# Performance work log

Measured on AMD Instinct MI355X. Metric: run time of the kernel, lower is better.

Reference implementation:

```python
import jax, jax.numpy as jnp
import numpy as np

B, N, D, H, L, R = 2, 1024, 128, 8, 8, 4
HD = D // H            # head dim = 16
DH = int(D * 2.0)      # mlp hidden (mlp_ratio=2.0)
TWO_R = 2 * R
LS_INIT = 1e-3


def _ln(x, g, b):
    m = x.mean(-1, keepdims=True)
    v = ((x - m) ** 2).mean(-1, keepdims=True)
    return (x - m) / jnp.sqrt(v + 1e-5) * g + b


def _gelu(t):
    return jax.nn.gelu(t, approximate=False)  # torch nn.GELU default (erf)


def _attn(x, mask, bias, qkv_w, proj_w, proj_b, w_pre, w_post):
    Bx, Nx, C = x.shape
    qkv = (x @ qkv_w.T).reshape(Bx, Nx, 3, H, HD).transpose(2, 0, 3, 1, 4)
    q, k, v = qkv[0], qkv[1], qkv[2]               # each [B,H,N,hd]
    a = jnp.einsum('bhid,bhjd->bhij', q, k) * (HD ** -0.5)
    a = a + mask[:, None] + bias                   # pairwise mask + rbf/edge bias
    a = jnp.einsum('bhij,gh->bgij', a, w_pre)      # talk-head pre-softmax
    a = jax.nn.softmax(a, axis=-1)
    a = jnp.einsum('bhij,gh->bgij', a, w_post)     # talk-head post-softmax
    o = jnp.einsum('bhij,bhjd->bihd', a, v).reshape(Bx, Nx, C)
    return o @ proj_w.T + proj_b


def setup_inputs() -> dict:
    key = jax.random.key(0)
    ks = jax.random.split(key, 16)
    s = 0.02
    x = jax.random.normal(ks[0], (B, N, D), jnp.float32)
    dist = jax.random.uniform(ks[1], (B, N, N), jnp.float32) * 20.0
    attn_mask = jnp.where(jax.random.uniform(ks[2], (B, N, N)) < 0.02, -1e4, 0.0).astype(jnp.float32)
    local_mask = jnp.where(dist > 8.0, -1e4, 0.0).astype(jnp.float32)
    edge_type = jax.random.randint(ks[3], (B, N, N), 0, 4)
    return {
        'x': x, 'dist': dist, 'attn_mask': attn_mask, 'local_mask': local_mask,
        'edge_type': edge_type,
        'ln_g': jnp.ones((L, 3, D), jnp.float32), 'ln_b': jnp.zeros((L, 3, D), jnp.float32),
        'qkv_w': jax.random.normal(ks[4], (L, 2, 3 * D, D), jnp.float32) * s,
        'proj_w': jax.random.normal(ks[5], (L, 2, D, D), jnp.float32) * s,
        'proj_b': jnp.zeros((L, 2, D), jnp.float32),
        'th_pre': jnp.eye(H, dtype=jnp.float32) + jax.random.normal(ks[6], (L, 2, H, H), jnp.float32) * s,
        'th_post': jnp.eye(H, dtype=jnp.float32) + jax.random.normal(ks[7], (L, 2, H, H), jnp.float32) * s,
        'ls': jnp.full((L, 3, D), LS_INIT, jnp.float32),
        'fc1_w': jax.random.normal(ks[8], (L, DH, D), jnp.float32) * s,
        'fc1_b': jnp.zeros((L, DH), jnp.float32),
        'fc2_w': jax.random.normal(ks[9], (L, D, DH), jnp.float32) * s,
        'fc2_b': jnp.zeros((L, D), jnp.float32),
        'de_ln_g': jnp.ones((L, TWO_R), jnp.float32), 'de_ln_b': jnp.zeros((L, TWO_R), jnp.float32),
        'de_w': jax.random.normal(ks[10], (L, H, TWO_R), jnp.float32) * 0.5,
        'de_b': jnp.zeros((L, H), jnp.float32),
        'edge_emb': jax.random.normal(ks[11], (L, 4, R), jnp.float32) * 0.5,
        'rbf_mu': jnp.linspace(0.0, 20.0, R).astype(jnp.float32),
        'rbf_sigma': jnp.full((R,), 20.0 / R, jnp.float32),
    }


def reference(x, dist, attn_mask, local_mask, edge_type, ln_g, ln_b, qkv_w, proj_w,
              proj_b, th_pre, th_post, ls, fc1_w, fc1_b, fc2_w, fc2_b,
              de_ln_g, de_ln_b, de_w, de_b, edge_emb, rbf_mu, rbf_sigma):
    # RBF features of pairwise distances: [B,N,N,R] (mu/sigma buffers shared across layers)
    rbf = jnp.exp(-(((dist[..., None] - rbf_mu) / rbf_sigma) ** 2))
    first_mask = attn_mask + local_mask  # num_dist_mask == 1
    for l in range(L):
        feat = jnp.concatenate([rbf, edge_emb[l][edge_type]], axis=-1)  # [B,N,N,2R]
        bias = _gelu(_ln(feat, de_ln_g[l], de_ln_b[l]) @ de_w[l].T + de_b[l])  # [B,N,N,H]
        bias = jnp.moveaxis(bias, -1, 1)  # [B,H,N,N]
        x = x + ls[l, 0] * _attn(_ln(x, ln_g[l, 0], ln_b[l, 0]), first_mask, bias,
                                 qkv_w[l, 0], proj_w[l, 0], proj_b[l, 0], th_pre[l, 0], th_post[l, 0])
        x = x + ls[l, 1] * _attn(_ln(x, ln_g[l, 1], ln_b[l, 1]), attn_mask, bias,
                                 qkv_w[l, 1], proj_w[l, 1], proj_b[l, 1], th_pre[l, 1], th_post[l, 1])
        h = _ln(x, ln_g[l, 2], ln_b[l, 2])
        h = _gelu(h @ fc1_w[l].T + fc1_b[l]) @ fc2_w[l].T + fc2_b[l]
        x = x + ls[l, 2] * h
    return x
```

## Files before the change

kernel.cpp:

```cpp
#include <hip/hip_runtime.h>
#include <math.h>

#define BB 2
#define NN 1024
#define DD 128
#define HH 8
#define NL 8
#define RR 4
#define DHID 256
#define TWO_R 8
#define MM (BB*NN)
#define TB 2048

typedef __attribute__((ext_vector_type(8))) short short8;
typedef __attribute__((ext_vector_type(4))) float f32x4;

__device__ __forceinline__ float gelu_erf(float x) {
    return 0.5f * x * (1.0f + erff(x * 0.70710678118654752f));
}
__device__ __forceinline__ ushort f2b(float f) {
    union { float f; unsigned u; } v; v.f = f;
    return (ushort)((v.u + 0x7FFFu + ((v.u >> 16) & 1u)) >> 16);
}
__device__ __forceinline__ float b2f(ushort u) {
    union { unsigned u; float f; } v; v.u = ((unsigned)u) << 16;
    return v.f;
}
__device__ __forceinline__ unsigned pk2(float a, float b) {
    return ((unsigned)f2b(b) << 16) | (unsigned)f2b(a);
}

__global__ __launch_bounds__(256) void cvt4_kernel(
    const float* __restrict__ s0, int n0, const float* __restrict__ s1, int n1,
    const float* __restrict__ s2, int n2, const float* __restrict__ s3, int n3,
    ushort* __restrict__ d0, ushort* __restrict__ d1,
    ushort* __restrict__ d2, ushort* __restrict__ d3) {
    int t = blockIdx.x * 256 + threadIdx.x;
    if (t < n0) { d0[t] = f2b(s0[t]); return; } t -= n0;
    if (t < n1) { d1[t] = f2b(s1[t]); return; } t -= n1;
    if (t < n2) { d2[t] = f2b(s2[t]); return; } t -= n2;
    if (t < n3) { d3[t] = f2b(s3[t]); }
}

__global__ __launch_bounds__(256) void maskprep_kernel(
    const float* __restrict__ am, const float* __restrict__ lm,
    ushort* __restrict__ fmask, ushort* __restrict__ amask) {
    int t = blockIdx.x * 256 + threadIdx.x;
    if (t >= BB * NN * NN) return;
    float a = am[t];
    amask[t] = f2b(a);
    fmask[t] = f2b(a + lm[t]);
}

__global__ __launch_bounds__(256) void table_kernel(
    const float* __restrict__ de_ln_g, const float* __restrict__ de_ln_b,
    const float* __restrict__ de_w, const float* __restrict__ de_b,
    const float* __restrict__ edge_emb, const float* __restrict__ mu,
    const float* __restrict__ sigma, float* __restrict__ tab) {
    int t = blockIdx.x * 256 + threadIdx.x;
    if (t >= NL * 4 * TB) return;
    int idx = t & (TB - 1);
    int et = (t >> 11) & 3;
    int l = t >> 13;
    float d = idx * (20.0f / (float)(TB - 1));
    float f[8];
#pragma unroll
    for (int r = 0; r < RR; ++r) {
        float u = (d - mu[r]) / sigma[r];
        f[r] = expf(-u * u);
    }
#pragma unroll
    for (int r = 0; r < RR; ++r) f[4 + r] = edge_emb[(l * 4 + et) * RR + r];
    float m = 0.f;
#pragma unroll
    for (int r = 0; r < 8; ++r) m += f[r];
    m *= 0.125f;
    float v = 0.f;
#pragma unroll
    for (int r = 0; r < 8; ++r) { float dd = f[r] - m; v += dd * dd; }
    v *= 0.125f;
    float inv = rsqrtf(v + 1e-5f);
    float fn[8];
#pragma unroll
    for (int r = 0; r < 8; ++r)
        fn[r] = (f[r] - m) * inv * de_ln_g[l * 8 + r] + de_ln_b[l * 8 + r];
#pragma unroll
    for (int h = 0; h < HH; ++h) {
        float z = de_b[l * 8 + h];
#pragma unroll
        for (int r = 0; r < 8; ++r) z += de_w[(l * 8 + h) * 8 + r] * fn[r];
        tab[(size_t)t * 8 + h] = gelu_erf(z);
    }
}

#define GF_BIAS 1
#define GF_GELU 2
#define GF_RESID 4
#define GF_OUTBF 8

template <int AMODE, int FLAGS, int KDIM>
__global__ __launch_bounds__(256) void gemm_mfma(
    const void* __restrict__ Ain, const ushort* __restrict__ W,
    const float* __restrict__ bias, const float* __restrict__ ls,
    const float* __restrict__ resid, const float* __restrict__ lng,
    const float* __restrict__ lnb, void* __restrict__ out, int Nd) {
    __shared__ ushort As[64][KDIM + 8];
    __shared__ ushort Ws[64][KDIM + 8];
    int tid = threadIdx.x;
    int bm = blockIdx.x, bn = blockIdx.y;
    if (AMODE == 1) {
        int r = tid >> 2, c = tid & 3;
        const float* xr = (const float*)Ain + (size_t)(bm * 64 + r) * 128 + c * 32;
        float v[32];
        float s = 0.f, ss = 0.f;
#pragma unroll
        for (int k = 0; k < 8; ++k) {
            float4 f = ((const float4*)xr)[k];
            v[4 * k] = f.x; v[4 * k + 1] = f.y; v[4 * k + 2] = f.z; v[4 * k + 3] = f.w;
            s += f.x + f.y + f.z + f.w;
            ss += f.x * f.x + f.y * f.y + f.z * f.z + f.w * f.w;
        }
        s += __shfl_xor(s, 1, 64);  s += __shfl_xor(s, 2, 64);
        ss += __shfl_xor(ss, 1, 64); ss += __shfl_xor(ss, 2, 64);
        float mean = s * (1.f / 128.f);
        float var = ss * (1.f / 128.f) - mean * mean;
        float inv = rsqrtf(var + 1e-5f);
        unsigned* dst = (unsigned*)&As[r][c * 32];
#pragma unroll
        for (int k = 0; k < 16; ++k) {
            int col = c * 32 + 2 * k;
            float a0 = (v[2 * k] - mean) * inv * lng[col] + lnb[col];
            float a1 = (v[2 * k + 1] - mean) * inv * lng[col + 1] + lnb[col + 1];
            dst[k] = pk2(a0, a1);
        }
    } else if (AMODE == 2) {
        const float* Apart = (const float*)Ain;
        for (int v = tid; v < 64 * 32; v += 256) {
            int r = v >> 5, c = v & 31;
            size_t off = (size_t)(bm * 64 + r) * 128 + c * 4;
            float4 s0 = *(const float4*)(Apart + off);
            float4 s1 = *(const float4*)(Apart + (size_t)MM * 128 + off);
            unsigned* dst = (unsigned*)&As[r][c * 4];
            dst[0] = pk2(s0.x + s1.x, s0.y + s1.y);
            dst[1] = pk2(s0.z + s1.z, s0.w + s1.w);
        }
    } else {
        const ushort* A = (const ushort*)Ain;
        for (int v = tid; v < 64 * KDIM / 8; v += 256) {
            int r = v / (KDIM / 8), c = v % (KDIM / 8);
            *(short8*)&As[r][c * 8] =
                *(const short8*)(A + (size_t)(bm * 64 + r) * KDIM + c * 8);
        }
    }
    for (int v = tid; v < 64 * KDIM / 8; v += 256) {
        int r = v / (KDIM / 8), c = v % (KDIM / 8);
        *(short8*)&Ws[r][c * 8] =
            *(const short8*)(W + (size_t)(bn * 64 + r) * KDIM + c * 8);
    }
    __syncthreads();
    int wv = tid >> 6, l = tid & 63;
    int wm = (wv >> 1) * 32, wn = (wv & 1) * 32;
    int lr = l & 15, lk = (l >> 4) * 8;
    f32x4 acc[2][2] = {};
#pragma unroll
    for (int k0 = 0; k0 < KDIM; k0 += 32) {
        short8 af[2], bf[2];
        af[0] = *(const short8*)&As[wm + lr][k0 + lk];
        af[1] = *(const short8*)&As[wm + 16 + lr][k0 + lk];
        bf[0] = *(const short8*)&Ws[wn + lr][k0 + lk];
        bf[1] = *(const short8*)&Ws[wn + 16 + lr][k0 + lk];
#pragma unroll
        for (int mf = 0; mf < 2; ++mf)
#pragma unroll
            for (int nf = 0; nf < 2; ++nf)
                acc[mf][nf] = __builtin_amdgcn_mfma_f32_16x16x32_bf16(
                    af[mf], bf[nf], acc[mf][nf], 0, 0, 0);
    }
#pragma unroll
    for (int mf = 0; mf < 2; ++mf)
#pragma unroll
        for (int nf = 0; nf < 2; ++nf) {
            int n = bn * 64 + wn + nf * 16 + lr;
            float bv = (FLAGS & GF_BIAS) ? bias[n] : 0.f;
            float lv = (FLAGS & GF_RESID) ? ls[n] : 0.f;
#pragma unroll
            for (int q = 0; q < 4; ++q) {
                int m = bm * 64 + wm + mf * 16 + (l >> 4) * 4 + q;
                float c = acc[mf][nf][q];
                c += bv;
                if (FLAGS & GF_GELU) c = gelu_erf(c);
                size_t idx = (size_t)m * Nd + n;
                if (FLAGS & GF_RESID) c = resid[idx] + lv * c;
                if (FLAGS & GF_OUTBF) ((ushort*)out)[idx] = f2b(c);
                else ((float*)out)[idx] = c;
            }
        }
}

__global__ __launch_bounds__(256) void score_mfma(
    const ushort* __restrict__ qkv, const float* __restrict__ dist,
    const int* __restrict__ edge_type, const float* __restrict__ tabl,
    const ushort* __restrict__ mask, ushort* __restrict__ a) {
    __shared__ unsigned bm2[4][1024];
    __shared__ ushort st[8][16][72];
    int tid = threadIdx.x, wv = tid >> 6, l = tid & 63;
    int jt = blockIdx.x, it = blockIdx.y, b = blockIdx.z;
    int i0 = it * 16, j0 = jt * 64;
    {
        int p0 = tid * 4;
        int il = p0 >> 6, jl = p0 & 63;
        size_t mi = ((size_t)(b * NN + i0 + il)) * NN + j0 + jl;
        float4 d4 = *(const float4*)(dist + mi);
        int4 e4 = *(const int4*)(edge_type + mi);
        uint2 mk = *(const uint2*)(mask + mi);
        float mk4[4] = { b2f((ushort)(mk.x & 0xFFFF)), b2f((ushort)(mk.x >> 16)),
                         b2f((ushort)(mk.y & 0xFFFF)), b2f((ushort)(mk.y >> 16)) };
        float dv[4] = { d4.x, d4.y, d4.z, d4.w };
        int ev[4] = { e4.x, e4.y, e4.z, e4.w };
        unsigned o[4][4];
#pragma unroll
        for (int p = 0; p < 4; ++p) {
            float u = dv[p] * ((float)(TB - 1) / 20.0f);
            int t0i = (int)u;
            t0i = t0i < 0 ? 0 : (t0i > TB - 2 ? TB - 2 : t0i);
            float fr = u - (float)t0i;
            const float* tp = tabl + ((size_t)ev[p] * TB + t0i) * 8;
            float4 lo0 = *(const float4*)tp;
            float4 lo1 = *(const float4*)(tp + 4);
            float4 hi0 = *(const float4*)(tp + 8);
            float4 hi1 = *(const float4*)(tp + 12);
            float m = mk4[p];
            o[p][0] = pk2(m + lo0.x + fr * (hi0.x - lo0.x),
                          m + lo0.y + fr * (hi0.y - lo0.y));
            o[p][1] = pk2(m + lo0.z + fr * (hi0.z - lo0.z),
                          m + lo0.w + fr * (hi0.w - lo0.w));
            o[p][2] = pk2(m + lo1.x + fr * (hi1.x - lo1.x),
                          m + lo1.y + fr * (hi1.y - lo1.y));
            o[p][3] = pk2(m + lo1.z + fr * (hi1.z - lo1.z),
                          m + lo1.w + fr * (hi1.w - lo1.w));
        }
#pragma unroll
        for (int hp = 0; hp < 4; ++hp) {
            uint4 w4;
            w4.x = o[0][hp]; w4.y = o[1][hp]; w4.z = o[2][hp]; w4.w = o[3][hp];
            *reinterpret_cast<uint4*>(&bm2[hp][p0]) = w4;
        }
    }
    int h0 = wv * 2;
    int lr = l & 15, kk = (l >> 4) * 8;
    short8 zero = {0, 0, 0, 0, 0, 0, 0, 0};
    bool lo = kk < 16;
    short8 af[2];
    short8 bf[2][4];
    f32x4 acc[2][4] = {};
#pragma unroll
    for (int hh = 0; hh < 2; ++hh) {
        af[hh] = zero;
        if (lo)
            af[hh] = *(const short8*)(qkv + (size_t)(b * NN + i0 + lr) * 384 +
                                      (h0 + hh) * 16 + kk);
#pragma unroll
        for (int nf = 0; nf < 4; ++nf) {
            bf[hh][nf] = zero;
            if (lo)
                bf[hh][nf] = *(const short8*)(qkv +
                                              (size_t)(b * NN + j0 + nf * 16 + lr) * 384 +
                                              128 + (h0 + hh) * 16 + kk);
        }
    }
#pragma unroll
    for (int hh = 0; hh < 2; ++hh)
#pragma unroll
        for (int nf = 0; nf < 4; ++nf)
            acc[hh][nf] = __builtin_amdgcn_mfma_f32_16x16x32_bf16(
                af[hh], bf[hh][nf], acc[hh][nf], 0, 0, 0);
    __syncthreads();
#pragma unroll
    for (int nf = 0; nf < 4; ++nf)
#pragma unroll
        for (int q = 0; q < 4; ++q) {
            int il = (l >> 4) * 4 + q;
            int jl = nf * 16 + lr;
            unsigned bmv = bm2[wv][il * 64 + jl];
            st[h0][il][jl]     = f2b(acc[0][nf][q] * 0.25f + b2f((ushort)(bmv & 0xFFFF)));
            st[h0 + 1][il][jl] = f2b(acc[1][nf][q] * 0.25f + b2f((ushort)(bmv >> 16)));
        }
    __syncthreads();
    {
        int row = tid >> 1;
        int h = row >> 4, il = row & 15;
        int jl = (tid & 1) * 32;
        const ushort* src = &st[h][il][jl];
        ushort* dst = a + ((size_t)(b * HH + h) * NN + i0 + il) * NN + j0 + jl;
        *reinterpret_cast<uint4*>(dst)      = *reinterpret_cast<const uint4*>(src);
        *reinterpret_cast<uint4*>(dst + 8)  = *reinterpret_cast<const uint4*>(src + 8);
        *reinterpret_cast<uint4*>(dst + 16) = *reinterpret_cast<const uint4*>(src + 16);
        *reinterpret_cast<uint4*>(dst + 24) = *reinterpret_cast<const uint4*>(src + 24);
    }
}

__global__ __launch_bounds__(256) void mixsm_kernel(
    ushort* __restrict__ a, const float* __restrict__ pre,
    const float* __restrict__ post) {
    __shared__ float red[8][4];
    int bi = blockIdx.x;
    int b = bi >> 10, i = bi & 1023;
    int tid = threadIdx.x, wave = tid >> 6, lane = tid & 63;
    float vals[8][4];
#pragma unroll
    for (int h = 0; h < HH; ++h) {
        uint2 w = *(const uint2*)(a + ((size_t)(b * HH + h) * NN + i) * NN + 4 * tid);
        vals[h][0] = b2f((ushort)(w.x & 0xFFFF));
        vals[h][1] = b2f((ushort)(w.x >> 16));
        vals[h][2] = b2f((ushort)(w.y & 0xFFFF));
        vals[h][3] = b2f((ushort)(w.y >> 16));
    }
    float e[8][4];
#pragma unroll
    for (int g = 0; g < HH; ++g) {
        float pr[8];
#pragma unroll
        for (int h = 0; h < 8; ++h) pr[h] = pre[g * 8 + h];
        float z = 0.f;
#pragma unroll
        for (int q = 0; q < 4; ++q) {
            float m = 0.f;
#pragma unroll
            for (int h = 0; h < 8; ++h) m += pr[h] * vals[h][q];
            e[g][q] = __expf(m);
            z += e[g][q];
        }
#pragma unroll
        for (int o = 32; o; o >>= 1) z += __shfl_xor(z, o, 64);
        if (lane == 0) red[g][wave] = z;
    }
    __syncthreads();
#pragma unroll
    for (int g = 0; g < HH; ++g) {
        float rz = 1.f / (red[g][0] + red[g][1] + red[g][2] + red[g][3]);
#pragma unroll
        for (int q = 0; q < 4; ++q) e[g][q] *= rz;
    }
#pragma unroll
    for (int g = 0; g < HH; ++g) {
        float po[8];
#pragma unroll
        for (int h = 0; h < 8; ++h) po[h] = post[g * 8 + h];
        float o4[4];
#pragma unroll
        for (int q = 0; q < 4; ++q) {
            float s = 0.f;
#pragma unroll
            for (int h = 0; h < 8; ++h) s += po[h] * e[h][q];
            o4[q] = s;
        }
        uint2 w;
        w.x = pk2(o4[0], o4[1]);
        w.y = pk2(o4[2], o4[3]);
        *(uint2*)(a + ((size_t)(b * HH + g) * NN + i) * NN + 4 * tid) = w;
    }
}

__global__ __launch_bounds__(256) void av_mfma(
    const ushort* __restrict__ p, const ushort* __restrict__ qkv,
    float* __restrict__ opart) {
    __shared__ ushort Vs[16][520];
    int bx = blockIdx.x;
    int it = bx >> 1, js = bx & 1;
    int bh = blockIdx.y;
    int b = bh >> 3, h = bh & 7;
    int tid = threadIdx.x, wv = tid >> 6, l = tid & 63;
    int i0 = it * 64 + wv * 16;
    int j0 = js * 512;
    for (int jl = tid; jl < 512; jl += 256) {
        const ushort* src = qkv + (size_t)(b * NN + j0 + jl) * 384 + 256 + h * 16;
        short8 v0 = *(const short8*)src;
        short8 v1 = *(const short8*)(src + 8);
#pragma unroll
        for (int d = 0; d < 8; ++d) Vs[d][jl] = (ushort)v0[d];
#pragma unroll
        for (int d = 0; d < 8; ++d) Vs[8 + d][jl] = (ushort)v1[d];
    }
    __syncthreads();
    int lr = l & 15, lk = (l >> 4) * 8;
    const ushort* prow = p + ((size_t)bh * NN + i0 + lr) * NN + j0;
    f32x4 acc0 = {}, acc1 = {};
#pragma unroll
    for (int ks = 0; ks < 16; ks += 2) {
        int jb0 = ks * 32 + lk;
        int jb1 = (ks + 1) * 32 + lk;
        short8 bv0 = *(const short8*)&Vs[lr][jb0];
        short8 bv1 = *(const short8*)&Vs[lr][jb1];
        short8 a0 = *(const short8*)(prow + jb0);
        short8 a1 = *(const short8*)(prow + jb1);
        acc0 = __builtin_amdgcn_mfma_f32_16x16x32_bf16(a0, bv0, acc0, 0, 0, 0);
        acc1 = __builtin_amdgcn_mfma_f32_16x16x32_bf16(a1, bv1, acc1, 0, 0, 0);
    }
    f32x4 acc = acc0 + acc1;
#pragma unroll
    for (int q = 0; q < 4; ++q) {
        int m = i0 + (l >> 4) * 4 + q;
        opart[((size_t)js * MM + b * NN + m) * DD + h * 16 + lr] = acc[q];
    }
}

extern "C" void kernel_launch(void* const* d_in, const int* in_sizes, int n_in,
                              void* d_out, int out_size, void* d_ws, size_t ws_size,
                              hipStream_t stream) {
    const float* x         = (const float*)d_in[0];
    const float* dist      = (const float*)d_in[1];
    const float* attn_mask = (const float*)d_in[2];
    const float* local_mask= (const float*)d_in[3];
    const int*   edge_type = (const int*)d_in[4];
    const float* ln_g      = (const float*)d_in[5];
    const float* ln_b      = (const float*)d_in[6];
    const float* qkv_w     = (const float*)d_in[7];
    const float* proj_w    = (const float*)d_in[8];
    const float* proj_b    = (const float*)d_in[9];
    const float* th_pre    = (const float*)d_in[10];
    const float* th_post   = (const float*)d_in[11];
    const float* ls        = (const float*)d_in[12];
    const float* fc1_w     = (const float*)d_in[13];
    const float* fc1_b     = (const float*)d_in[14];
    const float* fc2_w     = (const float*)d_in[15];
    const float* fc2_b     = (const float*)d_in[16];
    const float* de_ln_g   = (const float*)d_in[17];
    const float* de_ln_b   = (const float*)d_in[18];
    const float* de_w      = (const float*)d_in[19];
    const float* de_b      = (const float*)d_in[20];
    const float* edge_emb  = (const float*)d_in[21];
    const float* rbf_mu    = (const float*)d_in[22];
    const float* rbf_sigma = (const float*)d_in[23];

    char* pws = (char*)d_ws;
    auto alloc = [&](size_t bytes) {
        char* r = pws;
        pws += (bytes + 255) & ~(size_t)255;
        return (void*)r;
    };
    const int NWQ = NL * 2 * 3 * DD * DD;
    const int NWP = NL * 2 * DD * DD;
    const int NW1 = NL * DHID * DD;
    const int NW2 = NL * DD * DHID;
    ushort* wq    = (ushort*)alloc((size_t)NWQ * 2);
    ushort* wp    = (ushort*)alloc((size_t)NWP * 2);
    ushort* w1    = (ushort*)alloc((size_t)NW1 * 2);
    ushort* w2    = (ushort*)alloc((size_t)NW2 * 2);
    ushort* abuf  = (ushort*)alloc((size_t)BB * HH * NN * NN * 2);
    ushort* fmask = (ushort*)alloc((size_t)BB * NN * NN * 2);
    ushort* amask = (ushort*)alloc((size_t)BB * NN * NN * 2);
    float*  xbuf  = (float*)alloc((size_t)MM * DD * 4);
    ushort* qkvb  = (ushort*)alloc((size_t)MM * 3 * DD * 2);
    ushort* h1    = (ushort*)alloc((size_t)MM * DHID * 2);
    float*  opart = (float*)alloc((size_t)2 * MM * DD * 4);
    float*  tab   = (float*)alloc((size_t)NL * 4 * TB * 8 * 4);

    {
        int ntot = NWQ + NWP + NW1 + NW2;
        cvt4_kernel<<<(ntot + 255) / 256, 256, 0, stream>>>(
            qkv_w, NWQ, proj_w, NWP, fc1_w, NW1, fc2_w, NW2, wq, wp, w1, w2);
        maskprep_kernel<<<(BB * NN * NN + 255) / 256, 256, 0, stream>>>(
            attn_mask, local_mask, fmask, amask);
        table_kernel<<<(NL * 4 * TB + 255) / 256, 256, 0, stream>>>(
            de_ln_g, de_ln_b, de_w, de_b, edge_emb, rbf_mu, rbf_sigma, tab);
    }

    hipMemcpyAsync(xbuf, x, (size_t)MM * DD * 4, hipMemcpyDeviceToDevice, stream);

    for (int l = 0; l < NL; ++l) {
        const float* tabl = tab + (size_t)l * 4 * TB * 8;
        for (int inst = 0; inst < 2; ++inst) {
            gemm_mfma<1, GF_OUTBF, 128><<<dim3(MM / 64, 384 / 64), 256, 0, stream>>>(
                xbuf, wq + (size_t)(l * 2 + inst) * 3 * DD * DD,
                nullptr, nullptr, nullptr,
                ln_g + (l * 3 + inst) * DD, ln_b + (l * 3 + inst) * DD, qkvb, 384);
            score_mfma<<<dim3(NN / 64, NN / 16, BB), 256, 0, stream>>>(
                qkvb, dist, edge_type, tabl, inst == 0 ? fmask : amask, abuf);
            mixsm_kernel<<<BB * NN, 256, 0, stream>>>(
                abuf, th_pre + (l * 2 + inst) * HH * HH,
                th_post + (l * 2 + inst) * HH * HH);
            av_mfma<<<dim3(32, BB * HH), 256, 0, stream>>>(abuf, qkvb, opart);
            gemm_mfma<2, GF_BIAS | GF_RESID, 128>
                <<<dim3(MM / 64, DD / 64), 256, 0, stream>>>(
                opart, wp + (size_t)(l * 2 + inst) * DD * DD,
                proj_b + (l * 2 + inst) * DD, ls + (l * 3 + inst) * DD,
                xbuf, nullptr, nullptr, xbuf, DD);
        }

        gemm_mfma<1, GF_BIAS | GF_GELU | GF_OUTBF, 128>
            <<<dim3(MM / 64, DHID / 64), 256, 0, stream>>>(
            xbuf, w1 + (size_t)l * DHID * DD, fc1_b + l * DHID,
            nullptr, nullptr, ln_g + (l * 3 + 2) * DD, ln_b + (l * 3 + 2) * DD,
            h1, DHID);
        gemm_mfma<0, GF_BIAS | GF_RESID, 256>
            <<<dim3(MM / 64, DD / 64), 256, 0, stream>>>(
            h1, w2 + (size_t)l * DD * DHID, fc2_b + l * DD,
            ls + (l * 3 + 2) * DD, xbuf, nullptr, nullptr, xbuf, DD);
    }

    hipMemcpyAsync(d_out, xbuf, (size_t)MM * DD * 4, hipMemcpyDeviceToDevice, stream);
}
```

Before: 1.426 ms.

## Precompute per-layer bf16 pair bias once and stage Q/K tiles in LDS

Adds a per-layer kernel that interpolates the RBF/edge bias table once into a bf16 [B,N,N,H] buffer, so the two attention instances in a layer share it instead of each redoing the dist/edge_type gathers and interpolation. The score kernel now reads this precomputed bias and stages Q and K rows in shared memory with coalesced loads before the MFMA fragments are formed, reusing that LDS for the output staging. The trade is an extra write and read of a 32 MB bias buffer per layer against fewer scattered table reads and less arithmetic. It also adds a bf16 rounding step on the bias before the mask is added.

```diff
diff --git a/kernel.cpp b/kernel.cpp
--- a/kernel.cpp
+++ b/kernel.cpp
@@ -91,6 +91,30 @@
         for (int r = 0; r < 8; ++r) z += de_w[(l * 8 + h) * 8 + r] * fn[r];
         tab[(size_t)t * 8 + h] = gelu_erf(z);
     }
+}
+
+__global__ __launch_bounds__(256) void biasp_kernel(
+    const float* __restrict__ dist, const int* __restrict__ edge_type,
+    const float* __restrict__ tabl, ushort* __restrict__ biasp) {
+    int t = blockIdx.x * 256 + threadIdx.x;
+    if (t >= BB * NN * NN) return;
+    float d = dist[t];
+    int et = edge_type[t];
+    float u = d * ((float)(TB - 1) / 20.0f);
+    int t0i = (int)u;
+    t0i = t0i < 0 ? 0 : (t0i > TB - 2 ? TB - 2 : t0i);
+    float fr = u - (float)t0i;
+    const float* tp = tabl + ((size_t)et * TB + t0i) * 8;
+    float4 lo0 = *(const float4*)tp;
+    float4 lo1 = *(const float4*)(tp + 4);
+    float4 hi0 = *(const float4*)(tp + 8);
+    float4 hi1 = *(const float4*)(tp + 12);
+    uint4 w;
+    w.x = pk2(lo0.x + fr * (hi0.x - lo0.x), lo0.y + fr * (hi0.y - lo0.y));
+    w.y = pk2(lo0.z + fr * (hi0.z - lo0.z), lo0.w + fr * (hi0.w - lo0.w));
+    w.z = pk2(lo1.x + fr * (hi1.x - lo1.x), lo1.y + fr * (hi1.y - lo1.y));
+    w.w = pk2(lo1.z + fr * (hi1.z - lo1.z), lo1.w + fr * (hi1.w - lo1.w));
+    *reinterpret_cast<uint4*>(biasp + (size_t)t * 8) = w;
 }
 
 #define GF_BIAS 1
@@ -198,46 +222,42 @@
 }
 
 __global__ __launch_bounds__(256) void score_mfma(
-    const ushort* __restrict__ qkv, const float* __restrict__ dist,
-    const int* __restrict__ edge_type, const float* __restrict__ tabl,
+    const ushort* __restrict__ qkv, const ushort* __restrict__ biasp,
     const ushort* __restrict__ mask, ushort* __restrict__ a) {
+    __shared__ ushort Qs[16][136];
+    __shared__ ushort kst[9216];
     __shared__ unsigned bm2[4][1024];
-    __shared__ ushort st[8][16][72];
     int tid = threadIdx.x, wv = tid >> 6, l = tid & 63;
     int jt = blockIdx.x, it = blockIdx.y, b = blockIdx.z;
     int i0 = it * 16, j0 = jt * 64;
     {
+        int r = tid >> 4, c = tid & 15;
+        *(short8*)&Qs[r][c * 8] =
+            *(const short8*)(qkv + (size_t)(b * NN + i0 + r) * 384 + c * 8);
+    }
+#pragma unroll
+    for (int p = 0; p < 4; ++p) {
+        int cidx = p * 256 + tid;
+        int r = cidx >> 4, c = cidx & 15;
+        *(short8*)&kst[r * 136 + c * 8] =
+            *(const short8*)(qkv + (size_t)(b * NN + j0 + r) * 384 + 128 + c * 8);
+    }
+    {
         int p0 = tid * 4;
-        int il = p0 >> 6, jl = p0 & 63;
-        size_t mi = ((size_t)(b * NN + i0 + il)) * NN + j0 + jl;
-        float4 d4 = *(const float4*)(dist + mi);
-        int4 e4 = *(const int4*)(edge_type + mi);
+        size_t mi = ((size_t)(b * NN + i0 + (p0 >> 6))) * NN + j0 + (p0 & 63);
         uint2 mk = *(const uint2*)(mask + mi);
         float mk4[4] = { b2f((ushort)(mk.x & 0xFFFF)), b2f((ushort)(mk.x >> 16)),
                          b2f((ushort)(mk.y & 0xFFFF)), b2f((ushort)(mk.y >> 16)) };
-        float dv[4] = { d4.x, d4.y, d4.z, d4.w };
-        int ev[4] = { e4.x, e4.y, e4.z, e4.w };
         unsigned o[4][4];
 #pragma unroll
         for (int p = 0; p < 4; ++p) {
-            float u = dv[p] * ((float)(TB - 1) / 20.0f);
-            int t0i = (int)u;
-            t0i = t0i < 0 ? 0 : (t0i > TB - 2 ? TB - 2 : t0i);
-            float fr = u - (float)t0i;
-            const float* tp = tabl + ((size_t)ev[p] * TB + t0i) * 8;
-            float4 lo0 = *(const float4*)tp;
-            float4 lo1 = *(const float4*)(tp + 4);
-            float4 hi0 = *(const float4*)(tp + 8);
-            float4 hi1 = *(const float4*)(tp + 12);
+            uint4 bp = *reinterpret_cast<const uint4*>(biasp + (mi + p) * 8);
             float m = mk4[p];
-            o[p][0] = pk2(m + lo0.x + fr * (hi0.x - lo0.x),
-                          m + lo0.y + fr * (hi0.y - lo0.y));
-            o[p][1] = pk2(m + lo0.z + fr * (hi0.z - lo0.z),
-                          m + lo0.w + fr * (hi0.w - lo0.w));
-            o[p][2] = pk2(m + lo1.x + fr * (hi1.x - lo1.x),
-                          m + lo1.y + fr * (hi1.y - lo1.y));
-            o[p][3] = pk2(m + lo1.z + fr * (hi1.z - lo1.z),
-                          m + lo1.w + fr * (hi1.w - lo1.w));
+            unsigned wds[4] = { bp.x, bp.y, bp.z, bp.w };
+#pragma unroll
+            for (int hp = 0; hp < 4; ++hp)
+                o[p][hp] = pk2(b2f((ushort)(wds[hp] & 0xFFFF)) + m,
+                               b2f((ushort)(wds[hp] >> 16)) + m);
         }
 #pragma unroll
         for (int hp = 0; hp < 4; ++hp) {
@@ -246,6 +266,7 @@
             *reinterpret_cast<uint4*>(&bm2[hp][p0]) = w4;
         }
     }
+    __syncthreads();
     int h0 = wv * 2;
     int lr = l & 15, kk = (l >> 4) * 8;
     short8 zero = {0, 0, 0, 0, 0, 0, 0, 0};
@@ -256,16 +277,12 @@
 #pragma unroll
     for (int hh = 0; hh < 2; ++hh) {
         af[hh] = zero;
-        if (lo)
-            af[hh] = *(const short8*)(qkv + (size_t)(b * NN + i0 + lr) * 384 +
-                                      (h0 + hh) * 16 + kk);
+        if (lo) af[hh] = *(const short8*)&Qs[lr][(h0 + hh) * 16 + kk];
 #pragma unroll
         for (int nf = 0; nf < 4; ++nf) {
             bf[hh][nf] = zero;
-            if (lo)
-                bf[hh][nf] = *(const short8*)(qkv +
-                                              (size_t)(b * NN + j0 + nf * 16 + lr) * 384 +
-                                              128 + (h0 + hh) * 16 + kk);
+            if (lo) bf[hh][nf] =
+                *(const short8*)&kst[(nf * 16 + lr) * 136 + (h0 + hh) * 16 + kk];
         }
     }
 #pragma unroll
@@ -282,15 +299,17 @@
             int il = (l >> 4) * 4 + q;
             int jl = nf * 16 + lr;
             unsigned bmv = bm2[wv][il * 64 + jl];
-            st[h0][il][jl]     = f2b(acc[0][nf][q] * 0.25f + b2f((ushort)(bmv & 0xFFFF)));
-            st[h0 + 1][il][jl] = f2b(acc[1][nf][q] * 0.25f + b2f((ushort)(bmv >> 16)));
+            kst[(h0 * 16 + il) * 72 + jl] =
+                f2b(acc[0][nf][q] * 0.25f + b2f((ushort)(bmv & 0xFFFF)));
+            kst[((h0 + 1) * 16 + il) * 72 + jl] =
+                f2b(acc[1][nf][q] * 0.25f + b2f((ushort)(bmv >> 16)));
         }
     __syncthreads();
     {
         int row = tid >> 1;
         int h = row >> 4, il = row & 15;
         int jl = (tid & 1) * 32;
-        const ushort* src = &st[h][il][jl];
+        const ushort* src = &kst[(h * 16 + il) * 72 + jl];
         ushort* dst = a + ((size_t)(b * HH + h) * NN + i0 + il) * NN + j0 + jl;
         *reinterpret_cast<uint4*>(dst)      = *reinterpret_cast<const uint4*>(src);
         *reinterpret_cast<uint4*>(dst + 8)  = *reinterpret_cast<const uint4*>(src + 8);
@@ -447,6 +466,7 @@
     ushort* w1    = (ushort*)alloc((size_t)NW1 * 2);
     ushort* w2    = (ushort*)alloc((size_t)NW2 * 2);
     ushort* abuf  = (ushort*)alloc((size_t)BB * HH * NN * NN * 2);
+    ushort* biasp = (ushort*)alloc((size_t)BB * NN * NN * HH * 2);
     ushort* fmask = (ushort*)alloc((size_t)BB * NN * NN * 2);
     ushort* amask = (ushort*)alloc((size_t)BB * NN * NN * 2);
     float*  xbuf  = (float*)alloc((size_t)MM * DD * 4);
@@ -469,13 +489,15 @@
 
     for (int l = 0; l < NL; ++l) {
         const float* tabl = tab + (size_t)l * 4 * TB * 8;
+        biasp_kernel<<<(BB * NN * NN + 255) / 256, 256, 0, stream>>>(
+            dist, edge_type, tabl, biasp);
         for (int inst = 0; inst < 2; ++inst) {
             gemm_mfma<1, GF_OUTBF, 128><<<dim3(MM / 64, 384 / 64), 256, 0, stream>>>(
                 xbuf, wq + (size_t)(l * 2 + inst) * 3 * DD * DD,
                 nullptr, nullptr, nullptr,
                 ln_g + (l * 3 + inst) * DD, ln_b + (l * 3 + inst) * DD, qkvb, 384);
             score_mfma<<<dim3(NN / 64, NN / 16, BB), 256, 0, stream>>>(
-                qkvb, dist, edge_type, tabl, inst == 0 ? fmask : amask, abuf);
+                qkvb, biasp, inst == 0 ? fmask : amask, abuf);
             mixsm_kernel<<<BB * NN, 256, 0, stream>>>(
                 abuf, th_pre + (l * 2 + inst) * HH * HH,
                 th_post + (l * 2 + inst) * HH * HH);
```

New measurement: 1.315 ms. -7.8%, faster.
